# Performance work log

Hardware: AMD Instinct MI355X
Metric: run time of the kernel (lower is better)

Reference implementation:

```python
import jax, jax.numpy as jnp
import numpy as np

N = 2048          # nodes
IN_DIM = 512      # in_dim
H = 8             # num_heads
HD = IN_DIM // H  # head_dim = 64
L = 5             # max_path_len
E = 32768         # edges
D_EDGE = 64       # edge_feat_dim


def setup_inputs() -> dict:
    key = jax.random.key(0)
    ks = jax.random.split(key, 14)
    w = 1.0 / np.sqrt(IN_DIM)
    return {
        "node_feat": jax.random.normal(ks[0], (N, IN_DIM), jnp.float32),
        "edge_index": jax.random.randint(ks[1], (2, E), 0, N, dtype=jnp.int32),
        "max_path_len": 5,
        "shortest_distances": jax.random.randint(ks[2], (N, N), 0, L + 1, dtype=jnp.int32),
        "shortest_paths": jax.random.randint(ks[3], (N, N, L), 0, E + 1, dtype=jnp.int32),  # E == padding row
        "edge_feat": jax.random.normal(ks[4], (E, D_EDGE), jnp.float32),
        "attention_mask": jnp.zeros((N, N), jnp.int32),
        "WQ": jax.random.normal(ks[5], (IN_DIM, IN_DIM), jnp.float32) * w,
        "bQ": jax.random.normal(ks[6], (IN_DIM,), jnp.float32) * 0.02,
        "WK": jax.random.normal(ks[7], (IN_DIM, IN_DIM), jnp.float32) * w,
        "bK": jax.random.normal(ks[8], (IN_DIM,), jnp.float32) * 0.02,
        "WV": jax.random.normal(ks[9], (IN_DIM, IN_DIM), jnp.float32) * w,
        "bV": jax.random.normal(ks[10], (IN_DIM,), jnp.float32) * 0.02,
        "WO": jax.random.normal(ks[11], (IN_DIM, IN_DIM), jnp.float32) * w,
        "bO": jnp.zeros((IN_DIM,), jnp.float32),
        "spatial_bias": jax.random.normal(ks[12], ((L + 1) * H, 1), jnp.float32) * 0.02,
        "edge_weight": jax.random.normal(ks[13], ((L + 1) * H, D_EDGE), jnp.float32) * 0.02,
    }


def reference(node_feat, edge_index, max_path_len, shortest_distances, shortest_paths,
              edge_feat, attention_mask, WQ, bQ, WK, bK, WV, bV, WO, bO,
              spatial_bias, edge_weight):
    Nn, D = node_feat.shape
    Lp = max_path_len  # min(max_path_len, max_shortest_path_len); distances reach Lp here

    Q = (node_feat @ WQ + bQ).reshape(Nn, H, HD)
    K = (node_feat @ WK + bK).reshape(Nn, H, HD)
    V = (node_feat @ WV + bV).reshape(Nn, H, HD)

    # QK^T / sqrt(head_dim), laid out [N, N, H] as in the original after permute
    scores = jnp.einsum('nhd,mhd->nmh', Q, K) / np.sqrt(HD).astype(np.float32)

    # SpatialEncoding: bias table [(L+1)*H, 1] -> [L+1, H]; gather by clamped distance
    sp_table = spatial_bias.reshape(Lp + 1, H)
    dist = jnp.clip(shortest_distances, 0, Lp)
    scores = scores + sp_table[dist]  # [N, N, H]

    # EdgeEncoding: einsum('xyld,ldh->xyh') refactored as per-edge projection then gather
    W_e = edge_weight[: Lp * H].reshape(Lp, H, D_EDGE)  # (reshape[L,H,D].permute -> [L,D,H])
    padded = jnp.concatenate([edge_feat, jnp.zeros((1, D_EDGE), edge_feat.dtype)], axis=0)
    T = jnp.einsum('ed,lhd->elh', padded, W_e)  # [E+1, L, H]
    sp = shortest_paths[:, :, :Lp]
    gathered = T[sp, jnp.arange(Lp)[None, None, :]]  # [N, N, L, H]
    scores = scores + gathered.sum(axis=2)

    mask = attention_mask.astype(bool)
    scores = jnp.where(mask[:, :, None], -jnp.inf, scores)

    # NOTE: original applies softmax over dim=-1 of the [N, N, H] tensor (the head axis);
    # faithfully reproduced here. Dropout is identity (eval / p for inference).
    attn = jax.nn.softmax(scores, axis=-1)

    out = jnp.einsum('nmh,mhd->nhd', attn, V).reshape(Nn, D)
    return out @ WO + bO
```

## Files before the change

kernel.cpp:

```cpp
#include <hip/hip_runtime.h>

#define NN     2048
#define DIM    512
#define NH     8
#define HD     64
#define NE     32768
#define EPAD   32832
#define CHUNKS 8
#define CHSZ   (NN/CHUNKS)
#define NJT    (CHSZ/64)
#define QBLK   32
#define LOG2E  1.4426950408889634f

typedef __attribute__((ext_vector_type(8))) short bf16x8;
typedef __attribute__((ext_vector_type(4))) float f32x4;
typedef __attribute__((ext_vector_type(4))) unsigned int u32x4;

#define MFMA(a,b,c) __builtin_amdgcn_mfma_f32_16x16x32_bf16((a),(b),(c),0,0,0)

__device__ __forceinline__ float bf2f(unsigned int u16){
  union { unsigned int i; float f; } v; v.i = u16 << 16; return v.f;
}
__device__ __forceinline__ unsigned short f2bf(float f){
  union { float ff; unsigned int i; } v; v.ff = f;
  return (unsigned short)((v.i + 0x7fffu + ((v.i >> 16) & 1u)) >> 16);
}

__global__ __launch_bounds__(256) void prep_k(
    const float* __restrict__ X, const float* __restrict__ ef, const float* __restrict__ ew,
    unsigned short* __restrict__ Xb, unsigned short* __restrict__ pEF, unsigned short* __restrict__ pEW,
    const float* __restrict__ a0, const float* __restrict__ a1,
    const float* __restrict__ a2, const float* __restrict__ a3,
    unsigned short* __restrict__ Wt)
{
  __shared__ unsigned short tile[32][33];
  if (blockIdx.x < 1540){
    long g = (long)blockIdx.x*256 + threadIdx.x;
    const long GX = (long)NN*DIM/8;
    const long GE = (long)EPAD*8;
    const float* src; unsigned short* dst; long off, lim8;
    if (g < GX){ src = X;  dst = Xb;  off = g;        lim8 = GX; }
    else if (g < GX+GE){ src = ef; dst = pEF; off = g-GX; lim8 = (long)NE*8; }
    else { off = g-GX-GE; if (off >= 512) return; src = ew; dst = pEW; lim8 = 320; }
    unsigned short o[8];
    if (off < lim8){
      #pragma unroll
      for (int i=0;i<8;i++) o[i] = f2bf(src[off*8+i]);
    } else {
      #pragma unroll
      for (int i=0;i<8;i++) o[i] = 0;
    }
    *(uint4*)(dst + off*8) = *(const uint4*)o;
  } else {
    int b2 = blockIdx.x - 1540;
    int bz = b2 >> 8, rem = b2 & 255;
    int bx = (rem & 15)*32, by = (rem >> 4)*32;
    int tx = threadIdx.x & 31, ty = threadIdx.x >> 5;
    const float* src = bz==0 ? a0 : bz==1 ? a1 : bz==2 ? a2 : a3;
    unsigned short* dst = Wt + (size_t)bz*DIM*DIM;
    #pragma unroll
    for (int i=0;i<32;i+=8) tile[ty+i][tx] = f2bf(src[(size_t)(by+ty+i)*DIM + bx+tx]);
    __syncthreads();
    #pragma unroll
    for (int i=0;i<32;i+=8) dst[(size_t)(bx+ty+i)*DIM + by+tx] = tile[tx][ty+i];
  }
}

__global__ __launch_bounds__(256) void gemm_bt(
    const unsigned short* __restrict__ A1, const unsigned short* __restrict__ A2,
    const float* __restrict__ bias, unsigned short* __restrict__ C, float* __restrict__ Cf,
    int M, int N, int K, int bias_row)
{
  int lane = threadIdx.x & 63, w = threadIdx.x >> 6;
  int quad = lane >> 4, low = lane & 15;
  int m0 = blockIdx.y*64 + w*16;
  int n0 = blockIdx.x*32;
  f32x4 acc[2];
  acc[0] = (f32x4){0.f,0.f,0.f,0.f};
  acc[1] = (f32x4){0.f,0.f,0.f,0.f};
  #pragma unroll 4
  for (int k0=0; k0<K; k0+=32){
    bf16x8 a = *(const bf16x8*)(A1 + (size_t)(m0+low)*K + k0 + quad*8);
    #pragma unroll
    for (int t=0;t<2;t++){
      bf16x8 b = *(const bf16x8*)(A2 + (size_t)(n0+16*t+low)*K + k0 + quad*8);
      acc[t] = MFMA(a, b, acc[t]);
    }
  }
  #pragma unroll
  for (int t=0;t<2;t++){
    #pragma unroll
    for (int r=0;r<4;r++){
      int row = m0 + quad*4 + r;
      int col = n0 + 16*t + low;
      float v = acc[t][r];
      if (bias) v += bias[bias_row ? row : col];
      if (Cf) Cf[(size_t)row*N + col] = v;
      else    C [(size_t)row*N + col] = f2bf(v);
    }
  }
}

__global__ __launch_bounds__(256) void gemm_t2(
    const unsigned short* __restrict__ A1, const unsigned short* __restrict__ A2,
    unsigned short* __restrict__ T2L)
{
  int lane = threadIdx.x & 63, w = threadIdx.x >> 6;
  int quad = lane >> 4, low = lane & 15;
  int m0 = blockIdx.y*64 + w*16;
  int n0 = blockIdx.x*32;
  f32x4 acc[2];
  acc[0] = (f32x4){0.f,0.f,0.f,0.f};
  acc[1] = (f32x4){0.f,0.f,0.f,0.f};
  #pragma unroll
  for (int k0=0; k0<64; k0+=32){
    bf16x8 a = *(const bf16x8*)(A1 + (size_t)(m0+low)*64 + k0 + quad*8);
    #pragma unroll
    for (int t=0;t<2;t++){
      bf16x8 b = *(const bf16x8*)(A2 + (size_t)(n0+16*t+low)*64 + k0 + quad*8);
      acc[t] = MFMA(a, b, acc[t]);
    }
  }
  #pragma unroll
  for (int t=0;t<2;t++){
    #pragma unroll
    for (int r=0;r<4;r++){
      int row = m0 + quad*4 + r;
      int col = n0 + 16*t + low;
      T2L[((size_t)(col>>3)*EPAD + row)*8 + (col&7)] = f2bf(acc[t][r]);
    }
  }
}

__global__ __launch_bounds__(256) void biasqkv_k(
    const unsigned short* __restrict__ T2L, const float* __restrict__ spb,
    const int* __restrict__ dist, const int* __restrict__ sp, const int* __restrict__ maskp,
    unsigned short* __restrict__ biasB,
    const unsigned short* __restrict__ Xb, const unsigned short* __restrict__ Wt,
    const float* __restrict__ bQ, const float* __restrict__ bK, const float* __restrict__ bV,
    unsigned short* __restrict__ Qb, unsigned short* __restrict__ Kb, unsigned short* __restrict__ Vtb)
{
  __shared__ float sptab[48];
  if (blockIdx.x >= 512){
    if (threadIdx.x < 48) sptab[threadIdx.x] = spb[threadIdx.x];
    __syncthreads();
    long pix = (long)(blockIdx.x - 512)*256 + threadIdx.x;
    int dd = __builtin_nontemporal_load(dist + pix);
    int mk = __builtin_nontemporal_load(maskp + pix);
    int e[5];
    #pragma unroll
    for (int l=0;l<5;l++) e[l] = __builtin_nontemporal_load(sp + pix*5 + l);
    dd = dd < 0 ? 0 : (dd > 5 ? 5 : dd);
    float b[8];
    #pragma unroll
    for (int x=0;x<8;x++) b[x] = sptab[dd*8 + x];
    #pragma unroll
    for (int l=0;l<5;l++){
      int ee = e[l];
      if ((unsigned)ee > (unsigned)NE) ee = NE;
      uint4 tv = *(const uint4*)(T2L + ((size_t)l*EPAD + ee)*8);
      b[0] += bf2f(tv.x & 0xffffu); b[1] += bf2f(tv.x >> 16);
      b[2] += bf2f(tv.y & 0xffffu); b[3] += bf2f(tv.y >> 16);
      b[4] += bf2f(tv.z & 0xffffu); b[5] += bf2f(tv.z >> 16);
      b[6] += bf2f(tv.w & 0xffffu); b[7] += bf2f(tv.w >> 16);
    }
    unsigned short o[8];
    #pragma unroll
    for (int x=0;x<8;x++) o[x] = mk ? f2bf(-1e30f) : f2bf(b[x]);
    *(uint4*)(biasB + pix*8) = *(const uint4*)o;
  } else {
    int bid = blockIdx.x;
    int lane = threadIdx.x & 63, w = threadIdx.x >> 6;
    int quad = lane >> 4, low = lane & 15;
    int m0 = (bid >> 4)*64 + w*16;
    int n0 = (bid & 15)*32;
    f32x4 acc[3][2];
    #pragma unroll
    for (int z=0;z<3;z++){ acc[z][0]=(f32x4){0.f,0.f,0.f,0.f}; acc[z][1]=(f32x4){0.f,0.f,0.f,0.f}; }
    #pragma unroll 2
    for (int k0=0; k0<DIM; k0+=32){
      bf16x8 a = *(const bf16x8*)(Xb + (size_t)(m0+low)*DIM + k0 + quad*8);
      #pragma unroll
      for (int z=0;z<3;z++){
        #pragma unroll
        for (int t=0;t<2;t++){
          bf16x8 b = *(const bf16x8*)(Wt + (size_t)z*DIM*DIM + (size_t)(n0+16*t+low)*DIM + k0 + quad*8);
          acc[z][t] = MFMA(a, b, acc[z][t]);
        }
      }
    }
    #pragma unroll
    for (int t=0;t<2;t++){
      #pragma unroll
      for (int r=0;r<4;r++){
        int row = m0 + quad*4 + r;
        int col = n0 + 16*t + low;
        Qb[(size_t)row*DIM + col] = f2bf(acc[0][t][r] + bQ[col]);
        Kb[(size_t)row*DIM + col] = f2bf(acc[1][t][r] + bK[col]);
        Vtb[(size_t)col*NN + row] = f2bf(acc[2][t][r] + bV[col]);
      }
    }
  }
}

__global__ __launch_bounds__(512, 4) void attn_k(
    const unsigned short* __restrict__ Qb, const unsigned short* __restrict__ Kb,
    const unsigned short* __restrict__ Vt, const unsigned short* __restrict__ biasB,
    float* __restrict__ partO)
{
  __shared__ __attribute__((aligned(16))) float sld[NH][QBLK][68];
  unsigned int* p2 = (unsigned int*)sld;
  int tid = threadIdx.x;
  int lane = tid & 63, h = tid >> 6;
  int quad = lane >> 4, low = lane & 15;
  int q0 = blockIdx.x * QBLK;
  int chunk = blockIdx.y;

  bf16x8 aq[2][2];
  #pragma unroll
  for (int sq=0;sq<2;sq++)
    #pragma unroll
    for (int s=0;s<2;s++)
      aq[sq][s] = *(const bf16x8*)(Qb + (size_t)(q0+sq*16+low)*DIM + h*HD + s*32 + quad*8);

  f32x4 accO[2][4];
  #pragma unroll
  for (int sq=0;sq<2;sq++)
    #pragma unroll
    for (int t=0;t<4;t++) accO[sq][t] = (f32x4){0.f,0.f,0.f,0.f};

  uint4 pb[4];
  #pragma unroll
  for (int it=0; it<4; ++it){
    int p = tid + it*512;
    int qq = p >> 6, mm = p & 63;
    pb[it] = *(const uint4*)(biasB + ((size_t)(q0+qq)*NN + chunk*CHSZ + mm)*8);
  }

  for (int jt=0; jt<NJT; ++jt){
    int m0 = chunk*CHSZ + jt*64;

    f32x4 S[2][4];
    #pragma unroll
    for (int sq=0;sq<2;sq++)
      #pragma unroll
      for (int t=0;t<4;t++) S[sq][t] = (f32x4){0.f,0.f,0.f,0.f};
    #pragma unroll
    for (int s=0;s<2;s++){
      #pragma unroll
      for (int t=0;t<4;t++){
        bf16x8 bk = *(const bf16x8*)(Kb + (size_t)(m0+16*t+low)*DIM + h*HD + s*32 + quad*8);
        #pragma unroll
        for (int sq=0;sq<2;sq++)
          S[sq][t] = MFMA(aq[sq][s], bk, S[sq][t]);
      }
    }
    __syncthreads();

    #pragma unroll
    for (int sq=0;sq<2;sq++){
      #pragma unroll
      for (int t=0;t<4;t++){
        #pragma unroll
        for (int r=0;r<4;r++)
          sld[h][sq*16+quad*4+r][low+16*t] = S[sq][t][r]*0.125f;
      }
    }
    __syncthreads();

    #pragma unroll
    for (int it=0; it<4; ++it){
      int p = tid + it*512;
      int qq = p >> 6, mm = p & 63;
      uint4 tv = pb[it];
      float s0[8];
      s0[0] = sld[0][qq][mm] + bf2f(tv.x & 0xffffu);
      s0[1] = sld[1][qq][mm] + bf2f(tv.x >> 16);
      s0[2] = sld[2][qq][mm] + bf2f(tv.y & 0xffffu);
      s0[3] = sld[3][qq][mm] + bf2f(tv.y >> 16);
      s0[4] = sld[4][qq][mm] + bf2f(tv.z & 0xffffu);
      s0[5] = sld[5][qq][mm] + bf2f(tv.z >> 16);
      s0[6] = sld[6][qq][mm] + bf2f(tv.w & 0xffffu);
      s0[7] = sld[7][qq][mm] + bf2f(tv.w >> 16);
      float mx = s0[0];
      #pragma unroll
      for (int x=1;x<8;x++) mx = fmaxf(mx, s0[x]);
      float sum = 0.f;
      #pragma unroll
      for (int x=0;x<8;x++){ s0[x] = exp2f((s0[x]-mx)*LOG2E); sum += s0[x]; }
      float inv = (mx < -1e29f) ? 0.f : 1.f/sum;
      #pragma unroll
      for (int pr=0;pr<4;pr++){
        unsigned int u = (unsigned int)f2bf(s0[2*pr]*inv)
                       | ((unsigned int)f2bf(s0[2*pr+1]*inv) << 16);
        p2[pr*2176 + qq*68 + mm] = u;
      }
    }
    if (jt+1 < NJT){
      #pragma unroll
      for (int it=0; it<4; ++it){
        int p = tid + it*512;
        int qq = p >> 6, mm = p & 63;
        pb[it] = *(const uint4*)(biasB + ((size_t)(q0+qq)*NN + m0 + 64 + mm)*8);
      }
    }
    __syncthreads();

    bf16x8 ap[2][2];
    #pragma unroll
    for (int sq=0;sq<2;sq++){
      #pragma unroll
      for (int s=0;s<2;s++){
        const uint4* pp = (const uint4*)(p2 + (h>>1)*2176 + (size_t)(sq*16+low)*68 + s*32 + quad*8);
        uint4 w0 = pp[0], w1 = pp[1];
        bf16x8 a;
        if (h & 1){
          a[0]=(short)(w0.x>>16); a[1]=(short)(w0.y>>16); a[2]=(short)(w0.z>>16); a[3]=(short)(w0.w>>16);
          a[4]=(short)(w1.x>>16); a[5]=(short)(w1.y>>16); a[6]=(short)(w1.z>>16); a[7]=(short)(w1.w>>16);
        } else {
          a[0]=(short)(w0.x&0xffffu); a[1]=(short)(w0.y&0xffffu); a[2]=(short)(w0.z&0xffffu); a[3]=(short)(w0.w&0xffffu);
          a[4]=(short)(w1.x&0xffffu); a[5]=(short)(w1.y&0xffffu); a[6]=(short)(w1.z&0xffffu); a[7]=(short)(w1.w&0xffffu);
        }
        ap[sq][s] = a;
      }
    }
    #pragma unroll
    for (int s=0;s<2;s++){
      #pragma unroll
      for (int t=0;t<4;t++){
        bf16x8 bv = *(const bf16x8*)(Vt + (size_t)(h*HD + 16*t + low)*NN + m0 + s*32 + quad*8);
        #pragma unroll
        for (int sq=0;sq<2;sq++)
          accO[sq][t] = MFMA(ap[sq][s], bv, accO[sq][t]);
      }
    }
  }

  #pragma unroll
  for (int sq=0;sq<2;sq++){
    #pragma unroll
    for (int t=0;t<4;t++){
      #pragma unroll
      for (int r=0;r<4;r++){
        int q = sq*16 + quad*4 + r;
        partO[(((size_t)chunk*NN + q0 + q)*NH + h)*HD + 16*t + low] = accO[sq][t][r];
      }
    }
  }
}

__global__ __launch_bounds__(512) void merge_k(const float* __restrict__ partO,
                                               unsigned short* __restrict__ Obf)
{
  size_t idx = (size_t)blockIdx.x*512 + threadIdx.x;
  float s = 0.f;
  #pragma unroll
  for (int c=0;c<CHUNKS;c++) s += partO[(size_t)c*NN*DIM + idx];
  Obf[idx] = f2bf(s);
}

extern "C" void kernel_launch(void* const* d_in, const int* in_sizes, int n_in,
                              void* d_out, int out_size, void* d_ws, size_t ws_size,
                              hipStream_t stream)
{
  const float* X    = (const float*)d_in[0];
  const int*  dist  = (const int*)d_in[3];
  const int*  sp    = (const int*)d_in[4];
  const float* ef   = (const float*)d_in[5];
  const int*  maskp = (const int*)d_in[6];
  const float* WQ   = (const float*)d_in[7];
  const float* bQ   = (const float*)d_in[8];
  const float* WK   = (const float*)d_in[9];
  const float* bK   = (const float*)d_in[10];
  const float* WV   = (const float*)d_in[11];
  const float* bV   = (const float*)d_in[12];
  const float* WO   = (const float*)d_in[13];
  const float* bO   = (const float*)d_in[14];
  const float* spb  = (const float*)d_in[15];
  const float* ew   = (const float*)d_in[16];

  char* ws = (char*)d_ws;
  unsigned short* Wt   = (unsigned short*)(ws + 0);
  unsigned short* Xb   = (unsigned short*)(ws + 2097152);
  unsigned short* Qb   = (unsigned short*)(ws + 4194304);
  unsigned short* Kb   = (unsigned short*)(ws + 6291456);
  unsigned short* Vtb  = (unsigned short*)(ws + 8388608);
  unsigned short* pEF  = (unsigned short*)(ws + 10485760);
  unsigned short* pEW  = (unsigned short*)(ws + 14688256);
  unsigned short* T2L  = (unsigned short*)(ws + 14696448);
  unsigned short* Obf  = (unsigned short*)(ws + 18898944);
  unsigned short* biasB= (unsigned short*)(ws + 20996096);
  float*          pO   = (float*)(ws + 88104960);

  prep_k<<<dim3(2564), dim3(256), 0, stream>>>(X, ef, ew, Xb, pEF, pEW, WQ, WK, WV, WO, Wt);
  gemm_t2<<<dim3(2,513), dim3(256), 0, stream>>>(pEF, pEW, T2L);
  biasqkv_k<<<dim3(512 + NN*NN/256), dim3(256), 0, stream>>>(
      T2L, spb, dist, sp, maskp, biasB, Xb, Wt, bQ, bK, bV, Qb, Kb, Vtb);
  attn_k<<<dim3(NN/QBLK, CHUNKS), dim3(512), 0, stream>>>(Qb, Kb, Vtb, biasB, pO);
  merge_k<<<dim3(2048), dim3(512), 0, stream>>>(pO, Obf);
  gemm_bt<<<dim3(16,32), dim3(256), 0, stream>>>(Obf, Wt + 786432, bO, (unsigned short*)nullptr, (float*)d_out, NN, DIM, DIM, 0);
}
```

Before: 362.9 us.

## Split bias gather across kernels to overlap with first-half attention

The bias gather is split by key column: columns below 1280 are computed alongside the QKV projection, and the remaining columns are gathered inside a new kernel that also runs attention for the first four key chunks (which only need columns up to 1024). A second attention kernel then handles the last four chunks. Query block size drops from 32 to 16 and occupancy hints rise, so the gather's memory traffic can overlap attention compute. The trade-off is more launches, interleaved block roles, and halved Q reuse per block, which doubles K/V reads.

```diff
diff --git a/kernel.cpp b/kernel.cpp
--- a/kernel.cpp
+++ b/kernel.cpp
@@ -9,12 +9,11 @@
 #define CHUNKS 8
 #define CHSZ   (NN/CHUNKS)
 #define NJT    (CHSZ/64)
-#define QBLK   32
+#define QBLK   16
 #define LOG2E  1.4426950408889634f
 
 typedef __attribute__((ext_vector_type(8))) short bf16x8;
 typedef __attribute__((ext_vector_type(4))) float f32x4;
-typedef __attribute__((ext_vector_type(4))) unsigned int u32x4;
 
 #define MFMA(a,b,c) __builtin_amdgcn_mfma_f32_16x16x32_bf16((a),(b),(c),0,0,0)
 
@@ -132,106 +131,59 @@
   }
 }
 
-__global__ __launch_bounds__(256) void biasqkv_k(
-    const unsigned short* __restrict__ T2L, const float* __restrict__ spb,
-    const int* __restrict__ dist, const int* __restrict__ sp, const int* __restrict__ maskp,
-    unsigned short* __restrict__ biasB,
-    const unsigned short* __restrict__ Xb, const unsigned short* __restrict__ Wt,
-    const float* __restrict__ bQ, const float* __restrict__ bK, const float* __restrict__ bV,
-    unsigned short* __restrict__ Qb, unsigned short* __restrict__ Kb, unsigned short* __restrict__ Vtb)
-{
-  __shared__ float sptab[48];
-  if (blockIdx.x >= 512){
-    if (threadIdx.x < 48) sptab[threadIdx.x] = spb[threadIdx.x];
-    __syncthreads();
-    long pix = (long)(blockIdx.x - 512)*256 + threadIdx.x;
-    int dd = __builtin_nontemporal_load(dist + pix);
-    int mk = __builtin_nontemporal_load(maskp + pix);
-    int e[5];
-    #pragma unroll
-    for (int l=0;l<5;l++) e[l] = __builtin_nontemporal_load(sp + pix*5 + l);
-    dd = dd < 0 ? 0 : (dd > 5 ? 5 : dd);
-    float b[8];
-    #pragma unroll
-    for (int x=0;x<8;x++) b[x] = sptab[dd*8 + x];
-    #pragma unroll
-    for (int l=0;l<5;l++){
-      int ee = e[l];
-      if ((unsigned)ee > (unsigned)NE) ee = NE;
-      uint4 tv = *(const uint4*)(T2L + ((size_t)l*EPAD + ee)*8);
-      b[0] += bf2f(tv.x & 0xffffu); b[1] += bf2f(tv.x >> 16);
-      b[2] += bf2f(tv.y & 0xffffu); b[3] += bf2f(tv.y >> 16);
-      b[4] += bf2f(tv.z & 0xffffu); b[5] += bf2f(tv.z >> 16);
-      b[6] += bf2f(tv.w & 0xffffu); b[7] += bf2f(tv.w >> 16);
-    }
-    unsigned short o[8];
-    #pragma unroll
-    for (int x=0;x<8;x++) o[x] = mk ? f2bf(-1e30f) : f2bf(b[x]);
-    *(uint4*)(biasB + pix*8) = *(const uint4*)o;
-  } else {
-    int bid = blockIdx.x;
-    int lane = threadIdx.x & 63, w = threadIdx.x >> 6;
-    int quad = lane >> 4, low = lane & 15;
-    int m0 = (bid >> 4)*64 + w*16;
-    int n0 = (bid & 15)*32;
-    f32x4 acc[3][2];
-    #pragma unroll
-    for (int z=0;z<3;z++){ acc[z][0]=(f32x4){0.f,0.f,0.f,0.f}; acc[z][1]=(f32x4){0.f,0.f,0.f,0.f}; }
-    #pragma unroll 2
-    for (int k0=0; k0<DIM; k0+=32){
-      bf16x8 a = *(const bf16x8*)(Xb + (size_t)(m0+low)*DIM + k0 + quad*8);
-      #pragma unroll
-      for (int z=0;z<3;z++){
-        #pragma unroll
-        for (int t=0;t<2;t++){
-          bf16x8 b = *(const bf16x8*)(Wt + (size_t)z*DIM*DIM + (size_t)(n0+16*t+low)*DIM + k0 + quad*8);
-          acc[z][t] = MFMA(a, b, acc[z][t]);
-        }
-      }
-    }
-    #pragma unroll
-    for (int t=0;t<2;t++){
-      #pragma unroll
-      for (int r=0;r<4;r++){
-        int row = m0 + quad*4 + r;
-        int col = n0 + 16*t + low;
-        Qb[(size_t)row*DIM + col] = f2bf(acc[0][t][r] + bQ[col]);
-        Kb[(size_t)row*DIM + col] = f2bf(acc[1][t][r] + bK[col]);
-        Vtb[(size_t)col*NN + row] = f2bf(acc[2][t][r] + bV[col]);
-      }
-    }
-  }
-}
-
-__global__ __launch_bounds__(512, 4) void attn_k(
+__device__ __forceinline__ void gather_pair(long pix,
+    const unsigned short* __restrict__ T2L, const float* sptab,
+    const int* __restrict__ dist, const int* __restrict__ sp,
+    const int* __restrict__ maskp, unsigned short* __restrict__ biasB)
+{
+  int dd = __builtin_nontemporal_load(dist + pix);
+  int mk = __builtin_nontemporal_load(maskp + pix);
+  int e[5];
+  #pragma unroll
+  for (int l=0;l<5;l++) e[l] = __builtin_nontemporal_load(sp + pix*5 + l);
+  dd = dd < 0 ? 0 : (dd > 5 ? 5 : dd);
+  float b[8];
+  #pragma unroll
+  for (int x=0;x<8;x++) b[x] = sptab[dd*8 + x];
+  #pragma unroll
+  for (int l=0;l<5;l++){
+    int ee = e[l];
+    if ((unsigned)ee > (unsigned)NE) ee = NE;
+    uint4 tv = *(const uint4*)(T2L + ((size_t)l*EPAD + ee)*8);
+    b[0] += bf2f(tv.x & 0xffffu); b[1] += bf2f(tv.x >> 16);
+    b[2] += bf2f(tv.y & 0xffffu); b[3] += bf2f(tv.y >> 16);
+    b[4] += bf2f(tv.z & 0xffffu); b[5] += bf2f(tv.z >> 16);
+    b[6] += bf2f(tv.w & 0xffffu); b[7] += bf2f(tv.w >> 16);
+  }
+  unsigned short o[8];
+  #pragma unroll
+  for (int x=0;x<8;x++) o[x] = mk ? f2bf(-1e30f) : f2bf(b[x]);
+  *(uint4*)(biasB + pix*8) = *(const uint4*)o;
+}
+
+__device__ __forceinline__ void attn_tile(int q0, int chunk,
+    float (*sld)[QBLK][68],
     const unsigned short* __restrict__ Qb, const unsigned short* __restrict__ Kb,
     const unsigned short* __restrict__ Vt, const unsigned short* __restrict__ biasB,
     float* __restrict__ partO)
 {
-  __shared__ __attribute__((aligned(16))) float sld[NH][QBLK][68];
   unsigned int* p2 = (unsigned int*)sld;
   int tid = threadIdx.x;
   int lane = tid & 63, h = tid >> 6;
   int quad = lane >> 4, low = lane & 15;
-  int q0 = blockIdx.x * QBLK;
-  int chunk = blockIdx.y;
-
-  bf16x8 aq[2][2];
-  #pragma unroll
-  for (int sq=0;sq<2;sq++)
-    #pragma unroll
-    for (int s=0;s<2;s++)
-      aq[sq][s] = *(const bf16x8*)(Qb + (size_t)(q0+sq*16+low)*DIM + h*HD + s*32 + quad*8);
-
-  f32x4 accO[2][4];
-  #pragma unroll
-  for (int sq=0;sq<2;sq++)
-    #pragma unroll
-    for (int t=0;t<4;t++) accO[sq][t] = (f32x4){0.f,0.f,0.f,0.f};
-
-  uint4 pb[4];
-  #pragma unroll
-  for (int it=0; it<4; ++it){
+
+  bf16x8 aq[2];
+  #pragma unroll
+  for (int s=0;s<2;s++)
+    aq[s] = *(const bf16x8*)(Qb + (size_t)(q0+low)*DIM + h*HD + s*32 + quad*8);
+
+  f32x4 accO[4];
+  #pragma unroll
+  for (int t=0;t<4;t++) accO[t] = (f32x4){0.f,0.f,0.f,0.f};
+
+  uint4 pb[2];
+  #pragma unroll
+  for (int it=0; it<2; ++it){
     int p = tid + it*512;
     int qq = p >> 6, mm = p & 63;
     pb[it] = *(const uint4*)(biasB + ((size_t)(q0+qq)*NN + chunk*CHSZ + mm)*8);
@@ -240,36 +192,29 @@
   for (int jt=0; jt<NJT; ++jt){
     int m0 = chunk*CHSZ + jt*64;
 
-    f32x4 S[2][4];
-    #pragma unroll
-    for (int sq=0;sq<2;sq++)
-      #pragma unroll
-      for (int t=0;t<4;t++) S[sq][t] = (f32x4){0.f,0.f,0.f,0.f};
+    f32x4 S[4];
+    #pragma unroll
+    for (int t=0;t<4;t++) S[t] = (f32x4){0.f,0.f,0.f,0.f};
     #pragma unroll
     for (int s=0;s<2;s++){
       #pragma unroll
       for (int t=0;t<4;t++){
         bf16x8 bk = *(const bf16x8*)(Kb + (size_t)(m0+16*t+low)*DIM + h*HD + s*32 + quad*8);
-        #pragma unroll
-        for (int sq=0;sq<2;sq++)
-          S[sq][t] = MFMA(aq[sq][s], bk, S[sq][t]);
-      }
-    }
-    __syncthreads();
-
-    #pragma unroll
-    for (int sq=0;sq<2;sq++){
-      #pragma unroll
-      for (int t=0;t<4;t++){
-        #pragma unroll
-        for (int r=0;r<4;r++)
-          sld[h][sq*16+quad*4+r][low+16*t] = S[sq][t][r]*0.125f;
-      }
-    }
-    __syncthreads();
-
-    #pragma unroll
-    for (int it=0; it<4; ++it){
+        S[t] = MFMA(aq[s], bk, S[t]);
+      }
+    }
+    __syncthreads();
+
+    #pragma unroll
+    for (int t=0;t<4;t++){
+      #pragma unroll
+      for (int r=0;r<4;r++)
+        sld[h][quad*4+r][low+16*t] = S[t][r]*0.125f;
+    }
+    __syncthreads();
+
+    #pragma unroll
+    for (int it=0; it<2; ++it){
       int p = tid + it*512;
       int qq = p >> 6, mm = p & 63;
       uint4 tv = pb[it];
@@ -293,12 +238,12 @@
       for (int pr=0;pr<4;pr++){
         unsigned int u = (unsigned int)f2bf(s0[2*pr]*inv)
                        | ((unsigned int)f2bf(s0[2*pr+1]*inv) << 16);
-        p2[pr*2176 + qq*68 + mm] = u;
+        p2[pr*1088 + qq*68 + mm] = u;
       }
     }
     if (jt+1 < NJT){
       #pragma unroll
-      for (int it=0; it<4; ++it){
+      for (int it=0; it<2; ++it){
         int p = tid + it*512;
         int qq = p >> 6, mm = p & 63;
         pb[it] = *(const uint4*)(biasB + ((size_t)(q0+qq)*NN + m0 + 64 + mm)*8);
@@ -306,47 +251,123 @@
     }
     __syncthreads();
 
-    bf16x8 ap[2][2];
-    #pragma unroll
-    for (int sq=0;sq<2;sq++){
-      #pragma unroll
-      for (int s=0;s<2;s++){
-        const uint4* pp = (const uint4*)(p2 + (h>>1)*2176 + (size_t)(sq*16+low)*68 + s*32 + quad*8);
-        uint4 w0 = pp[0], w1 = pp[1];
-        bf16x8 a;
-        if (h & 1){
-          a[0]=(short)(w0.x>>16); a[1]=(short)(w0.y>>16); a[2]=(short)(w0.z>>16); a[3]=(short)(w0.w>>16);
-          a[4]=(short)(w1.x>>16); a[5]=(short)(w1.y>>16); a[6]=(short)(w1.z>>16); a[7]=(short)(w1.w>>16);
-        } else {
-          a[0]=(short)(w0.x&0xffffu); a[1]=(short)(w0.y&0xffffu); a[2]=(short)(w0.z&0xffffu); a[3]=(short)(w0.w&0xffffu);
-          a[4]=(short)(w1.x&0xffffu); a[5]=(short)(w1.y&0xffffu); a[6]=(short)(w1.z&0xffffu); a[7]=(short)(w1.w&0xffffu);
-        }
-        ap[sq][s] = a;
-      }
+    bf16x8 ap[2];
+    #pragma unroll
+    for (int s=0;s<2;s++){
+      const uint4* pp = (const uint4*)(p2 + (h>>1)*1088 + (size_t)low*68 + s*32 + quad*8);
+      uint4 w0 = pp[0], w1 = pp[1];
+      bf16x8 a;
+      if (h & 1){
+        a[0]=(short)(w0.x>>16); a[1]=(short)(w0.y>>16); a[2]=(short)(w0.z>>16); a[3]=(short)(w0.w>>16);
+        a[4]=(short)(w1.x>>16); a[5]=(short)(w1.y>>16); a[6]=(short)(w1.z>>16); a[7]=(short)(w1.w>>16);
+      } else {
+        a[0]=(short)(w0.x&0xffffu); a[1]=(short)(w0.y&0xffffu); a[2]=(short)(w0.z&0xffffu); a[3]=(short)(w0.w&0xffffu);
+        a[4]=(short)(w1.x&0xffffu); a[5]=(short)(w1.y&0xffffu); a[6]=(short)(w1.z&0xffffu); a[7]=(short)(w1.w&0xffffu);
+      }
+      ap[s] = a;
     }
     #pragma unroll
     for (int s=0;s<2;s++){
       #pragma unroll
       for (int t=0;t<4;t++){
         bf16x8 bv = *(const bf16x8*)(Vt + (size_t)(h*HD + 16*t + low)*NN + m0 + s*32 + quad*8);
+        accO[t] = MFMA(ap[s], bv, accO[t]);
+      }
+    }
+  }
+
+  #pragma unroll
+  for (int t=0;t<4;t++){
+    #pragma unroll
+    for (int r=0;r<4;r++){
+      int q = quad*4 + r;
+      partO[(((size_t)chunk*NN + q0 + q)*NH + h)*HD + 16*t + low] = accO[t][r];
+    }
+  }
+}
+
+__global__ __launch_bounds__(512, 8) void qkvgather_k(
+    const unsigned short* __restrict__ T2L, const float* __restrict__ spb,
+    const int* __restrict__ dist, const int* __restrict__ sp, const int* __restrict__ maskp,
+    unsigned short* __restrict__ biasB,
+    const unsigned short* __restrict__ Xb, const unsigned short* __restrict__ Wt,
+    const float* __restrict__ bQ, const float* __restrict__ bK, const float* __restrict__ bV,
+    unsigned short* __restrict__ Qb, unsigned short* __restrict__ Kb, unsigned short* __restrict__ Vtb)
+{
+  __shared__ float sptab[48];
+  if (blockIdx.x < 256){
+    int bid = blockIdx.x;
+    int lane = threadIdx.x & 63, w = threadIdx.x >> 6;
+    int quad = lane >> 4, low = lane & 15;
+    int m0 = (bid >> 3)*64 + (w & 3)*16;
+    int n0 = (bid & 7)*64 + (w >> 2)*32;
+    f32x4 acc[3][2];
+    #pragma unroll
+    for (int z=0;z<3;z++){ acc[z][0]=(f32x4){0.f,0.f,0.f,0.f}; acc[z][1]=(f32x4){0.f,0.f,0.f,0.f}; }
+    #pragma unroll 2
+    for (int k0=0; k0<DIM; k0+=32){
+      bf16x8 a = *(const bf16x8*)(Xb + (size_t)(m0+low)*DIM + k0 + quad*8);
+      #pragma unroll
+      for (int z=0;z<3;z++){
         #pragma unroll
-        for (int sq=0;sq<2;sq++)
-          accO[sq][t] = MFMA(ap[sq][s], bv, accO[sq][t]);
-      }
-    }
-  }
-
-  #pragma unroll
-  for (int sq=0;sq<2;sq++){
-    #pragma unroll
-    for (int t=0;t<4;t++){
+        for (int t=0;t<2;t++){
+          bf16x8 b = *(const bf16x8*)(Wt + (size_t)z*DIM*DIM + (size_t)(n0+16*t+low)*DIM + k0 + quad*8);
+          acc[z][t] = MFMA(a, b, acc[z][t]);
+        }
+      }
+    }
+    #pragma unroll
+    for (int t=0;t<2;t++){
       #pragma unroll
       for (int r=0;r<4;r++){
-        int q = sq*16 + quad*4 + r;
-        partO[(((size_t)chunk*NN + q0 + q)*NH + h)*HD + 16*t + low] = accO[sq][t][r];
-      }
-    }
-  }
+        int row = m0 + quad*4 + r;
+        int col = n0 + 16*t + low;
+        Qb[(size_t)row*DIM + col] = f2bf(acc[0][t][r] + bQ[col]);
+        Kb[(size_t)row*DIM + col] = f2bf(acc[1][t][r] + bK[col]);
+        Vtb[(size_t)col*NN + row] = f2bf(acc[2][t][r] + bV[col]);
+      }
+    }
+  } else {
+    if (threadIdx.x < 48) sptab[threadIdx.x] = spb[threadIdx.x];
+    __syncthreads();
+    unsigned int idx = (blockIdx.x - 256)*512u + threadIdx.x;
+    unsigned int n = idx / 1280u;
+    unsigned int m = idx - n*1280u;
+    gather_pair((long)n*NN + m, T2L, sptab, dist, sp, maskp, biasB);
+  }
+}
+
+__global__ __launch_bounds__(512, 8) void attngather_k(
+    const unsigned short* __restrict__ Qb, const unsigned short* __restrict__ Kb,
+    const unsigned short* __restrict__ Vt, const unsigned short* __restrict__ biasB,
+    float* __restrict__ partO,
+    const unsigned short* __restrict__ T2L, const float* __restrict__ spb,
+    const int* __restrict__ dist, const int* __restrict__ sp, const int* __restrict__ maskp,
+    unsigned short* __restrict__ biasW)
+{
+  __shared__ __attribute__((aligned(16))) float sld[NH][QBLK][68];
+  __shared__ float sptab[48];
+  if (blockIdx.x < 1024 && !(blockIdx.x & 1)){
+    int aid = blockIdx.x >> 1;
+    attn_tile((aid & 127)*16, aid >> 7, sld, Qb, Kb, Vt, biasB, partO);
+  } else {
+    int gid = (blockIdx.x < 1024) ? (int)(blockIdx.x >> 1) : (int)(blockIdx.x - 512);
+    if (threadIdx.x < 48) sptab[threadIdx.x] = spb[threadIdx.x];
+    __syncthreads();
+    unsigned int idx = (unsigned int)gid*512u + threadIdx.x;
+    unsigned int n = idx / 768u;
+    unsigned int m = 1280u + (idx - n*768u);
+    gather_pair((long)n*NN + m, T2L, sptab, dist, sp, maskp, biasW);
+  }
+}
+
+__global__ __launch_bounds__(512, 4) void attn2_k(
+    const unsigned short* __restrict__ Qb, const unsigned short* __restrict__ Kb,
+    const unsigned short* __restrict__ Vt, const unsigned short* __restrict__ biasB,
+    float* __restrict__ partO)
+{
+  __shared__ __attribute__((aligned(16))) float sld[NH][QBLK][68];
+  attn_tile(blockIdx.x*16, 4 + blockIdx.y, sld, Qb, Kb, Vt, biasB, partO);
 }
 
 __global__ __launch_bounds__(512) void merge_k(const float* __restrict__ partO,
@@ -394,9 +415,11 @@
 
   prep_k<<<dim3(2564), dim3(256), 0, stream>>>(X, ef, ew, Xb, pEF, pEW, WQ, WK, WV, WO, Wt);
   gemm_t2<<<dim3(2,513), dim3(256), 0, stream>>>(pEF, pEW, T2L);
-  biasqkv_k<<<dim3(512 + NN*NN/256), dim3(256), 0, stream>>>(
+  qkvgather_k<<<dim3(256 + 5120), dim3(512), 0, stream>>>(
       T2L, spb, dist, sp, maskp, biasB, Xb, Wt, bQ, bK, bV, Qb, Kb, Vtb);
-  attn_k<<<dim3(NN/QBLK, CHUNKS), dim3(512), 0, stream>>>(Qb, Kb, Vtb, biasB, pO);
+  attngather_k<<<dim3(1024 + 2560), dim3(512), 0, stream>>>(
+      Qb, Kb, Vtb, biasB, pO, T2L, spb, dist, sp, maskp, biasB);
+  attn2_k<<<dim3(128, 4), dim3(512), 0, stream>>>(Qb, Kb, Vtb, biasB, pO);
   merge_k<<<dim3(2048), dim3(512), 0, stream>>>(pO, Obf);
   gemm_bt<<<dim3(16,32), dim3(256), 0, stream>>>(Obf, Wt + 786432, bO, (unsigned short*)nullptr, (float*)d_out, NN, DIM, DIM, 0);
 }
```

After: 444.5 us. +22.5%, slower.

## Halve attention query block to 16 rows and use nontemporal bias loads

Applied to the files above, without the earlier changes.

Shrinks the attention kernel's query block from 32 to 16 rows, which halves the register footprint per thread and its shared-memory tile. The launch bound changes from 4 to 8 blocks per CU to raise occupancy. The bias tensor is now read with nontemporal loads so this streaming data does not pollute the cache. The cost is twice as many blocks, and each K/V tile loaded from global memory is reused across fewer query rows.

```diff
diff --git a/kernel.cpp b/kernel.cpp
--- a/kernel.cpp
+++ b/kernel.cpp
@@ -9,7 +9,7 @@
 #define CHUNKS 8
 #define CHSZ   (NN/CHUNKS)
 #define NJT    (CHSZ/64)
-#define QBLK   32
+#define QBLK   16
 #define LOG2E  1.4426950408889634f
 
 typedef __attribute__((ext_vector_type(8))) short bf16x8;
@@ -203,7 +203,7 @@
   }
 }
 
-__global__ __launch_bounds__(512, 4) void attn_k(
+__global__ __launch_bounds__(512, 8) void attn_k(
     const unsigned short* __restrict__ Qb, const unsigned short* __restrict__ Kb,
     const unsigned short* __restrict__ Vt, const unsigned short* __restrict__ biasB,
     float* __restrict__ partO)
@@ -216,72 +216,62 @@
   int q0 = blockIdx.x * QBLK;
   int chunk = blockIdx.y;
 
-  bf16x8 aq[2][2];
-  #pragma unroll
-  for (int sq=0;sq<2;sq++)
-    #pragma unroll
-    for (int s=0;s<2;s++)
-      aq[sq][s] = *(const bf16x8*)(Qb + (size_t)(q0+sq*16+low)*DIM + h*HD + s*32 + quad*8);
-
-  f32x4 accO[2][4];
-  #pragma unroll
-  for (int sq=0;sq<2;sq++)
-    #pragma unroll
-    for (int t=0;t<4;t++) accO[sq][t] = (f32x4){0.f,0.f,0.f,0.f};
-
-  uint4 pb[4];
-  #pragma unroll
-  for (int it=0; it<4; ++it){
+  bf16x8 aq[2];
+  #pragma unroll
+  for (int s=0;s<2;s++)
+    aq[s] = *(const bf16x8*)(Qb + (size_t)(q0+low)*DIM + h*HD + s*32 + quad*8);
+
+  f32x4 accO[4];
+  #pragma unroll
+  for (int t=0;t<4;t++) accO[t] = (f32x4){0.f,0.f,0.f,0.f};
+
+  u32x4 pb[2];
+  #pragma unroll
+  for (int it=0; it<2; ++it){
     int p = tid + it*512;
     int qq = p >> 6, mm = p & 63;
-    pb[it] = *(const uint4*)(biasB + ((size_t)(q0+qq)*NN + chunk*CHSZ + mm)*8);
+    pb[it] = __builtin_nontemporal_load(
+        (const u32x4*)(biasB + ((size_t)(q0+qq)*NN + chunk*CHSZ + mm)*8));
   }
 
   for (int jt=0; jt<NJT; ++jt){
     int m0 = chunk*CHSZ + jt*64;
 
-    f32x4 S[2][4];
-    #pragma unroll
-    for (int sq=0;sq<2;sq++)
-      #pragma unroll
-      for (int t=0;t<4;t++) S[sq][t] = (f32x4){0.f,0.f,0.f,0.f};
+    f32x4 S[4];
+    #pragma unroll
+    for (int t=0;t<4;t++) S[t] = (f32x4){0.f,0.f,0.f,0.f};
     #pragma unroll
     for (int s=0;s<2;s++){
       #pragma unroll
       for (int t=0;t<4;t++){
         bf16x8 bk = *(const bf16x8*)(Kb + (size_t)(m0+16*t+low)*DIM + h*HD + s*32 + quad*8);
-        #pragma unroll
-        for (int sq=0;sq<2;sq++)
-          S[sq][t] = MFMA(aq[sq][s], bk, S[sq][t]);
-      }
-    }
-    __syncthreads();
-
-    #pragma unroll
-    for (int sq=0;sq<2;sq++){
-      #pragma unroll
-      for (int t=0;t<4;t++){
-        #pragma unroll
-        for (int r=0;r<4;r++)
-          sld[h][sq*16+quad*4+r][low+16*t] = S[sq][t][r]*0.125f;
-      }
-    }
-    __syncthreads();
-
-    #pragma unroll
-    for (int it=0; it<4; ++it){
+        S[t] = MFMA(aq[s], bk, S[t]);
+      }
+    }
+    __syncthreads();
+
+    #pragma unroll
+    for (int t=0;t<4;t++){
+      #pragma unroll
+      for (int r=0;r<4;r++)
+        sld[h][quad*4+r][low+16*t] = S[t][r]*0.125f;
+    }
+    __syncthreads();
+
+    #pragma unroll
+    for (int it=0; it<2; ++it){
       int p = tid + it*512;
       int qq = p >> 6, mm = p & 63;
-      uint4 tv = pb[it];
+      u32x4 tv = pb[it];
       float s0[8];
-      s0[0] = sld[0][qq][mm] + bf2f(tv.x & 0xffffu);
-      s0[1] = sld[1][qq][mm] + bf2f(tv.x >> 16);
-      s0[2] = sld[2][qq][mm] + bf2f(tv.y & 0xffffu);
-      s0[3] = sld[3][qq][mm] + bf2f(tv.y >> 16);
-      s0[4] = sld[4][qq][mm] + bf2f(tv.z & 0xffffu);
-      s0[5] = sld[5][qq][mm] + bf2f(tv.z >> 16);
-      s0[6] = sld[6][qq][mm] + bf2f(tv.w & 0xffffu);
-      s0[7] = sld[7][qq][mm] + bf2f(tv.w >> 16);
+      s0[0] = sld[0][qq][mm] + bf2f(tv[0] & 0xffffu);
+      s0[1] = sld[1][qq][mm] + bf2f(tv[0] >> 16);
+      s0[2] = sld[2][qq][mm] + bf2f(tv[1] & 0xffffu);
+      s0[3] = sld[3][qq][mm] + bf2f(tv[1] >> 16);
+      s0[4] = sld[4][qq][mm] + bf2f(tv[2] & 0xffffu);
+      s0[5] = sld[5][qq][mm] + bf2f(tv[2] >> 16);
+      s0[6] = sld[6][qq][mm] + bf2f(tv[3] & 0xffffu);
+      s0[7] = sld[7][qq][mm] + bf2f(tv[3] >> 16);
       float mx = s0[0];
       #pragma unroll
       for (int x=1;x<8;x++) mx = fmaxf(mx, s0[x]);
@@ -293,58 +283,51 @@
       for (int pr=0;pr<4;pr++){
         unsigned int u = (unsigned int)f2bf(s0[2*pr]*inv)
                        | ((unsigned int)f2bf(s0[2*pr+1]*inv) << 16);
-        p2[pr*2176 + qq*68 + mm] = u;
+        p2[pr*1088 + qq*68 + mm] = u;
       }
     }
     if (jt+1 < NJT){
       #pragma unroll
-      for (int it=0; it<4; ++it){
+      for (int it=0; it<2; ++it){
         int p = tid + it*512;
         int qq = p >> 6, mm = p & 63;
-        pb[it] = *(const uint4*)(biasB + ((size_t)(q0+qq)*NN + m0 + 64 + mm)*8);
-      }
-    }
-    __syncthreads();
-
-    bf16x8 ap[2][2];
-    #pragma unroll
-    for (int sq=0;sq<2;sq++){
-      #pragma unroll
-      for (int s=0;s<2;s++){
-        const uint4* pp = (const uint4*)(p2 + (h>>1)*2176 + (size_t)(sq*16+low)*68 + s*32 + quad*8);
-        uint4 w0 = pp[0], w1 = pp[1];
-        bf16x8 a;
-        if (h & 1){
-          a[0]=(short)(w0.x>>16); a[1]=(short)(w0.y>>16); a[2]=(short)(w0.z>>16); a[3]=(short)(w0.w>>16);
-          a[4]=(short)(w1.x>>16); a[5]=(short)(w1.y>>16); a[6]=(short)(w1.z>>16); a[7]=(short)(w1.w>>16);
-        } else {
-          a[0]=(short)(w0.x&0xffffu); a[1]=(short)(w0.y&0xffffu); a[2]=(short)(w0.z&0xffffu); a[3]=(short)(w0.w&0xffffu);
-          a[4]=(short)(w1.x&0xffffu); a[5]=(short)(w1.y&0xffffu); a[6]=(short)(w1.z&0xffffu); a[7]=(short)(w1.w&0xffffu);
-        }
-        ap[sq][s] = a;
-      }
+        pb[it] = __builtin_nontemporal_load(
+            (const u32x4*)(biasB + ((size_t)(q0+qq)*NN + m0 + 64 + mm)*8));
+      }
+    }
+    __syncthreads();
+
+    bf16x8 ap[2];
+    #pragma unroll
+    for (int s=0;s<2;s++){
+      const uint4* pp = (const uint4*)(p2 + (h>>1)*1088 + (size_t)low*68 + s*32 + quad*8);
+      uint4 w0 = pp[0], w1 = pp[1];
+      bf16x8 a;
+      if (h & 1){
+        a[0]=(short)(w0.x>>16); a[1]=(short)(w0.y>>16); a[2]=(short)(w0.z>>16); a[3]=(short)(w0.w>>16);
+        a[4]=(short)(w1.x>>16); a[5]=(short)(w1.y>>16); a[6]=(short)(w1.z>>16); a[7]=(short)(w1.w>>16);
+      } else {
+        a[0]=(short)(w0.x&0xffffu); a[1]=(short)(w0.y&0xffffu); a[2]=(short)(w0.z&0xffffu); a[3]=(short)(w0.w&0xffffu);
+        a[4]=(short)(w1.x&0xffffu); a[5]=(short)(w1.y&0xffffu); a[6]=(short)(w1.z&0xffffu); a[7]=(short)(w1.w&0xffffu);
+      }
+      ap[s] = a;
     }
     #pragma unroll
     for (int s=0;s<2;s++){
       #pragma unroll
       for (int t=0;t<4;t++){
         bf16x8 bv = *(const bf16x8*)(Vt + (size_t)(h*HD + 16*t + low)*NN + m0 + s*32 + quad*8);
-        #pragma unroll
-        for (int sq=0;sq<2;sq++)
-          accO[sq][t] = MFMA(ap[sq][s], bv, accO[sq][t]);
-      }
-    }
-  }
-
-  #pragma unroll
-  for (int sq=0;sq<2;sq++){
-    #pragma unroll
-    for (int t=0;t<4;t++){
-      #pragma unroll
-      for (int r=0;r<4;r++){
-        int q = sq*16 + quad*4 + r;
-        partO[(((size_t)chunk*NN + q0 + q)*NH + h)*HD + 16*t + low] = accO[sq][t][r];
-      }
+        accO[t] = MFMA(ap[s], bv, accO[t]);
+      }
+    }
+  }
+
+  #pragma unroll
+  for (int t=0;t<4;t++){
+    #pragma unroll
+    for (int r=0;r<4;r++){
+      int q = quad*4 + r;
+      partO[(((size_t)chunk*NN + q0 + q)*NH + h)*HD + 16*t + low] = accO[t][r];
     }
   }
 }
```

After: 393.1 us. +8.3%, slower.
